# Kernel optimization log

Hardware: AMD Instinct MI355X
Metric: run time of the kernel (lower is better)

Reference implementation:

```python
import jax, jax.numpy as jnp
import numpy as np

HIDDEN = 1024
HEADS = 16
HEAD_DIM = HIDDEN // HEADS  # 64
BATCH = 2
SEQ = 2048
MASK_IDENTITY = True


def setup_inputs() -> dict:
    key = jax.random.key(0)
    ks = jax.random.split(key, 9)
    s = 1.0 / np.sqrt(HIDDEN)
    return {
        "hidden_states": jax.random.normal(ks[0], (BATCH, SEQ, HIDDEN), jnp.float32),
        "Wq": jax.random.normal(ks[1], (HIDDEN, HIDDEN), jnp.float32) * s,
        "bq": jnp.zeros((HIDDEN,), jnp.float32),
        "Wk": jax.random.normal(ks[2], (HIDDEN, HIDDEN), jnp.float32) * s,
        "bk": jnp.zeros((HIDDEN,), jnp.float32),
        "Wv": jax.random.normal(ks[3], (HIDDEN, HIDDEN), jnp.float32) * s,
        "bv": jnp.zeros((HIDDEN,), jnp.float32),
        "Wd": jax.random.normal(ks[4], (HIDDEN, HIDDEN), jnp.float32) * s,
        "bd": jnp.zeros((HIDDEN,), jnp.float32),
    }


def _split_heads(x):
    # [B, S, H*Dh] -> [B, H, S, Dh]
    b, s, _ = x.shape
    return x.reshape(b, s, HEADS, HEAD_DIM).transpose(0, 2, 1, 3)


def reference(hidden_states, Wq, bq, Wk, bk, Wv, bv, Wd, bd):
    # torch Linear: y = x @ W.T + b
    q = _split_heads(hidden_states @ Wq.T + bq)  # [B,H,S,Dh]
    k = _split_heads(hidden_states @ Wk.T + bk)
    v = _split_heads(hidden_states @ Wv.T + bv)

    scores = jnp.einsum("bhqd,bhkd->bhqk", q, k) / np.sqrt(HEAD_DIM)
    if MASK_IDENTITY:
        mask_value = -jnp.finfo(scores.dtype).max
        eye = jnp.eye(scores.shape[-1], dtype=bool)  # [S,S], broadcast over B,H
        scores = jnp.where(eye, mask_value, scores)
    probs = jax.nn.softmax(scores, axis=-1)
    ctx = jnp.einsum("bhqk,bhkd->bhqd", probs, v)  # [B,H,S,Dh]
    b, h, s, d = ctx.shape
    ctx = ctx.transpose(0, 2, 1, 3).reshape(b, s, h * d)  # [B,S,H*Dh]
    return ctx @ Wd.T + bd
```

## Files before the change

kernel.cpp:

```cpp
#include <hip/hip_runtime.h>
#include <hip/hip_bf16.h>
#include <stdint.h>

#define HIDDEN 1024
#define SEQL   2048
#define NB     2
#define NH     16
#define DH     64
#define MTOT   (NB * SEQL)
#define QKVLD  3072
#define SCALE_Q 0.18033688011112042f

typedef __bf16 bf16x8 __attribute__((ext_vector_type(8)));
typedef __bf16 bf16x4 __attribute__((ext_vector_type(4)));
typedef float  f32x4  __attribute__((ext_vector_type(4)));
typedef float  f32x16 __attribute__((ext_vector_type(16)));

__device__ __forceinline__ void gload16(const void* g, void* l) {
    __builtin_amdgcn_global_load_lds(
        (const __attribute__((address_space(1))) void*)g,
        (__attribute__((address_space(3))) void*)l, 16, 0, 0);
}
__device__ __forceinline__ float exp2fast(float x) {
    float r;
    asm("v_exp_f32 %0, %1" : "=v"(r) : "v"(x));
    return r;
}
__device__ __forceinline__ unsigned cvtpk(float lo, float hi) {
    unsigned r;
    asm("v_cvt_pk_bf16_f32 %0, %1, %2" : "=v"(r) : "v"(lo), "v"(hi));
    return r;
}
__device__ __forceinline__ void pswap(unsigned& a, unsigned& b) {
    asm volatile("v_permlane32_swap_b32 %0, %1" : "+v"(a), "+v"(b));
}
__device__ __forceinline__ void barrier_vm4() {
    asm volatile("s_waitcnt vmcnt(4)" ::: "memory");
    __builtin_amdgcn_s_barrier();
    asm volatile("" ::: "memory");
}

__global__ void prep(const float* __restrict__ H,
                     const float* __restrict__ Wq, const float* __restrict__ Wk,
                     const float* __restrict__ Wv, const float* __restrict__ Wd,
                     const float* __restrict__ bq, const float* __restrict__ bk,
                     const float* __restrict__ bv,
                     __bf16* __restrict__ Hb, __bf16* __restrict__ Wall,
                     float* __restrict__ bqkv) {
    const int bid = blockIdx.x, tid = threadIdx.x;
    if (bid < 4096) {
        int i = bid * 256 + tid;
        float4 v = reinterpret_cast<const float4*>(H)[i];
        bf16x4 o = { (__bf16)v.x, (__bf16)v.y, (__bf16)v.z, (__bf16)v.w };
        reinterpret_cast<bf16x4*>(Hb)[i] = o;
    } else if (bid < 8192) {
        int wi = bid - 4096;
        int seg = wi >> 10;
        int i = (wi & 1023) * 256 + tid;
        const float* src = seg == 0 ? Wq : seg == 1 ? Wk : seg == 2 ? Wv : Wd;
        float sc = (seg == 0) ? SCALE_Q : 1.0f;
        float4 v = reinterpret_cast<const float4*>(src)[i];
        bf16x4 o = { (__bf16)(v.x * sc), (__bf16)(v.y * sc),
                     (__bf16)(v.z * sc), (__bf16)(v.w * sc) };
        reinterpret_cast<bf16x4*>(Wall)[(size_t)seg * 262144 + i] = o;
    } else {
        for (int i = tid; i < 3072; i += 256) {
            float v = (i < 1024) ? bq[i] * SCALE_Q
                    : (i < 2048) ? bk[i - 1024] : bv[i - 2048];
            bqkv[i] = v;
        }
    }
}

__global__ __launch_bounds__(256) void transpose_v(const __bf16* __restrict__ QKV,
                                                   __bf16* __restrict__ Vt) {
    __shared__ __bf16 t[64][66];
    const int st = blockIdx.x, bh = blockIdx.y;
    const int b = bh >> 4, h = bh & 15;
    const int tid = threadIdx.x;
    const int r = tid >> 3, c = tid & 7;
    const __bf16* src = QKV + (size_t)(b * SEQL + st * 64) * QKVLD + 2048 + h * 64;
    *(int4*)&t[r][c * 8]      = *(const int4*)(src + (size_t)r * QKVLD + c * 8);
    *(int4*)&t[r + 32][c * 8] = *(const int4*)(src + (size_t)(r + 32) * QKVLD + c * 8);
    __syncthreads();
    __bf16* dst = Vt + (size_t)bh * DH * SEQL + st * 64;
    const int d = tid >> 3;
    __bf16 tmp0[8], tmp1[8];
#pragma unroll
    for (int j = 0; j < 8; ++j) {
        tmp0[j] = t[c * 8 + j][d];
        tmp1[j] = t[c * 8 + j][d + 32];
    }
    *(int4*)(dst + (size_t)d * SEQL + c * 8)        = *(int4*)tmp0;
    *(int4*)(dst + (size_t)(d + 32) * SEQL + c * 8) = *(int4*)tmp1;
}

__global__ __launch_bounds__(256) void gemm_qkv(const __bf16* __restrict__ A,
                                                const __bf16* __restrict__ Bw,
                                                const float* __restrict__ bias,
                                                __bf16* __restrict__ C) {
    __shared__ __bf16 As[3][128 * 32];
    __shared__ __bf16 Bs[3][128 * 32];
    const int K = 1024, N = QKVLD;

    int bid = blockIdx.x;
    int swz = (bid & 7) * 96 + (bid >> 3);
    const int bm = (swz & 31) * 128;
    const int bn = (swz >> 5) * 128;

    const int tid = threadIdx.x;
    const int w = tid >> 6, l = tid & 63, g = l >> 4, lc = l & 15;
    const int wr = (w >> 1) * 64, wc = (w & 1) * 64;
    const int row = tid >> 2, ch = tid & 3;

    const __bf16* Ap = A  + (size_t)(bm + row) * K + ch * 8;
    const __bf16* Bp = Bw + (size_t)(bn + row) * K + ch * 8;

    auto gstage = [&](int kt, int slot) {
        gload16(Ap + kt,                   &As[slot][w * 512]);
        gload16(Ap + kt + (size_t)64 * K,  &As[slot][2048 + w * 512]);
        gload16(Bp + kt,                   &Bs[slot][w * 512]);
        gload16(Bp + kt + (size_t)64 * K,  &Bs[slot][2048 + w * 512]);
    };

    f32x4 acc[4][4];
    const f32x4 z4 = {0.f, 0.f, 0.f, 0.f};
#pragma unroll
    for (int i = 0; i < 4; ++i)
#pragma unroll
        for (int j = 0; j < 4; ++j) acc[i][j] = z4;

    gstage(0, 0);
    gstage(32, 1);

    for (int kt = 0, it = 0; kt < K; kt += 32, ++it) {
        barrier_vm4();
        if (kt + 64 < K) gstage(kt + 64, (it + 2) % 3);

        const __bf16* Asl = &As[it % 3][0];
        const __bf16* Bsl = &Bs[it % 3][0];
        bf16x8 af[4], bfr[4];
#pragma unroll
        for (int i = 0; i < 4; ++i)
            af[i] = *(const bf16x8*)&Asl[(wr + i * 16 + lc) * 32 + g * 8];
#pragma unroll
        for (int j = 0; j < 4; ++j)
            bfr[j] = *(const bf16x8*)&Bsl[(wc + j * 16 + lc) * 32 + g * 8];
        __builtin_amdgcn_s_setprio(1);
#pragma unroll
        for (int i = 0; i < 4; ++i)
#pragma unroll
            for (int j = 0; j < 4; ++j)
                acc[i][j] = __builtin_amdgcn_mfma_f32_16x16x32_bf16(af[i], bfr[j], acc[i][j], 0, 0, 0);
        __builtin_amdgcn_s_setprio(0);
    }

#pragma unroll
    for (int i = 0; i < 4; ++i) {
        int r0 = bm + wr + i * 16 + g * 4;
#pragma unroll
        for (int j = 0; j < 4; ++j) {
            int c = bn + wc + j * 16 + lc;
            float bb = bias[c];
#pragma unroll
            for (int r = 0; r < 4; ++r)
                C[(size_t)(r0 + r) * N + c] = (__bf16)(acc[i][j][r] + bb);
        }
    }
}

__global__ __launch_bounds__(256) void gemm_out(const __bf16* __restrict__ A,
                                                const __bf16* __restrict__ Bw,
                                                const float* __restrict__ bias,
                                                float* __restrict__ Cout) {
    __shared__ __bf16 As[64 * 32];
    __shared__ __bf16 Bs[128 * 32];
    const int K = 1024, N = 1024;

    int bid = blockIdx.x;
    int swz = (bid & 7) * 64 + (bid >> 3);
    const int bm = (swz & 63) * 64;
    const int bn = (swz >> 6) * 128;

    const int tid = threadIdx.x;
    const int w = tid >> 6, l = tid & 63, g = l >> 4, lc = l & 15;
    const int wr = (w >> 1) * 32, wc = (w & 1) * 64;
    const int row = tid >> 2, ch = tid & 3;

    const __bf16* Ap = A  + (size_t)(bm + row) * K + ch * 8;
    const __bf16* Bp = Bw + (size_t)(bn + row) * K + ch * 8;
    __bf16* AsW  = &As[w * 512];
    __bf16* BsLo = &Bs[w * 512];
    __bf16* BsHi = &Bs[2048 + w * 512];

    f32x4 acc[2][4];
    const f32x4 z4 = {0.f, 0.f, 0.f, 0.f};
#pragma unroll
    for (int i = 0; i < 2; ++i)
#pragma unroll
        for (int j = 0; j < 4; ++j) acc[i][j] = z4;

    for (int kt = 0; kt < K; kt += 32) {
        gload16(Ap + kt,                   AsW);
        gload16(Bp + kt,                   BsLo);
        gload16(Bp + kt + (size_t)64 * K,  BsHi);
        __syncthreads();

        bf16x8 af[2], bfr[4];
#pragma unroll
        for (int i = 0; i < 2; ++i)
            af[i] = *(const bf16x8*)&As[(wr + i * 16 + lc) * 32 + g * 8];
#pragma unroll
        for (int j = 0; j < 4; ++j)
            bfr[j] = *(const bf16x8*)&Bs[(wc + j * 16 + lc) * 32 + g * 8];
        __builtin_amdgcn_s_setprio(1);
#pragma unroll
        for (int i = 0; i < 2; ++i)
#pragma unroll
            for (int j = 0; j < 4; ++j)
                acc[i][j] = __builtin_amdgcn_mfma_f32_16x16x32_bf16(af[i], bfr[j], acc[i][j], 0, 0, 0);
        __builtin_amdgcn_s_setprio(0);
        __syncthreads();
    }

#pragma unroll
    for (int i = 0; i < 2; ++i) {
        int r0 = bm + wr + i * 16 + g * 4;
#pragma unroll
        for (int j = 0; j < 4; ++j) {
            int c = bn + wc + j * 16 + lc;
            float bb = bias[c];
#pragma unroll
            for (int r = 0; r < 4; ++r)
                Cout[(size_t)(r0 + r) * N + c] = acc[i][j][r] + bb;
        }
    }
}

__global__ __launch_bounds__(512) void attn_kernel(const __bf16* __restrict__ QKV,
                                                   const __bf16* __restrict__ Vt,
                                                   __bf16* __restrict__ Ctx) {
    __shared__ __bf16 k_lds[3][128][64];
    __shared__ __bf16 v_lds[3][64][128];
    __shared__ float  bc[8][32];

    const int tid = threadIdx.x;
    const int w  = tid >> 6;
    const int l  = tid & 63;
    const int ql = l & 31;
    const int lh = l >> 5;

    int bid = blockIdx.x;
    int swz = (bid & 7) * 32 + (bid >> 3);
    const int qt = swz & 7, bh = swz >> 3;
    const int b = bh >> 4, hd = bh & 15;
    const int qw = qt * 256 + w * 32;

    const __bf16* Qg = QKV + (size_t)b * SEQL * QKVLD + hd * DH;
    const __bf16* Kg = Qg + 1024;
    const __bf16* Vg = Vt + (size_t)bh * DH * SEQL;

    bf16x8 qf[4];
    {
        const __bf16* qp = Qg + (size_t)(qw + ql) * QKVLD + lh * 8;
#pragma unroll
        for (int c = 0; c < 4; ++c) qf[c] = *(const bf16x8*)(qp + c * 16);
    }

    const int sr   = l >> 3;
    const int gcol = ((l & 7) ^ sr) * 8;
    const int vr  = l >> 4;
    const int vch = l & 15;
    auto stage = [&](int kb, int slot) {
        gload16(Kg + (size_t)(kb + w * 8 + sr) * QKVLD + gcol,      &k_lds[slot][w * 8][0]);
        gload16(Kg + (size_t)(kb + 64 + w * 8 + sr) * QKVLD + gcol, &k_lds[slot][64 + w * 8][0]);
        int dr0 = w * 4 + vr;
        int dr1 = 32 + w * 4 + vr;
        gload16(Vg + (size_t)dr0 * SEQL + kb + (vch ^ (dr0 & 7)) * 8, &v_lds[slot][w * 4][0]);
        gload16(Vg + (size_t)dr1 * SEQL + kb + (vch ^ (dr1 & 7)) * 8, &v_lds[slot][32 + w * 4][0]);
    };

    f32x16 o0, o1;
#pragma unroll
    for (int r = 0; r < 16; ++r) { o0[r] = 0.f; o1[r] = 0.f; }
    float l8[8];
#pragma unroll
    for (int r = 0; r < 8; ++r) l8[r] = 0.f;

    f32x16 zc;
#pragma unroll
    for (int r = 0; r < 16; ++r) zc[r] = 0.f;

    const int NT = SEQL / 128;
    const int rsw = (ql & 7) << 3;

    stage(0, 0);
    stage(128, 1);

    for (int kt = 0; kt < NT; ++kt) {
        barrier_vm4();
        if (kt + 2 < NT) stage((kt + 2) * 128, (kt + 2) % 3);

        const int buf = kt % 3;
        const int kb = kt * 128;

#pragma unroll
        for (int sub = 0; sub < 2; ++sub) {
            const int kbs = kb + sub * 64;
            const int ro  = sub * 64;

            f32x16 sA, sB;
            __builtin_amdgcn_s_setprio(1);
            {
                bf16x8 k0 = *(const bf16x8*)&k_lds[buf][ro + ql]     [(lh * 8) ^ rsw];
                bf16x8 k1 = *(const bf16x8*)&k_lds[buf][ro + 32 + ql][(lh * 8) ^ rsw];
                sA = __builtin_amdgcn_mfma_f32_32x32x16_bf16(k0, qf[0], zc, 0, 0, 0);
                sB = __builtin_amdgcn_mfma_f32_32x32x16_bf16(k1, qf[0], zc, 0, 0, 0);
            }
#pragma unroll
            for (int c = 1; c < 4; ++c) {
                bf16x8 k0 = *(const bf16x8*)&k_lds[buf][ro + ql]     [(c * 16 + lh * 8) ^ rsw];
                bf16x8 k1 = *(const bf16x8*)&k_lds[buf][ro + 32 + ql][(c * 16 + lh * 8) ^ rsw];
                sA = __builtin_amdgcn_mfma_f32_32x32x16_bf16(k0, qf[c], sA, 0, 0, 0);
                sB = __builtin_amdgcn_mfma_f32_32x32x16_bf16(k1, qf[c], sB, 0, 0, 0);
            }
            __builtin_amdgcn_s_setprio(0);

            if (kbs < qw + 32 && qw < kbs + 64) {
                const int qg = qw + ql;
#pragma unroll
                for (int i = 0; i < 16; ++i) {
                    int kg = kbs + (i & 3) + ((i >> 2) & 3) * 8 + lh * 4;
                    if (kg == qg)      sA[i] = -1e30f;
                    if (kg + 32 == qg) sB[i] = -1e30f;
                }
            }

#pragma unroll
            for (int i = 0; i < 16; ++i) sA[i] = exp2fast(sA[i]);
#pragma unroll
            for (int i = 0; i < 16; ++i) sB[i] = exp2fast(sB[i]);
#pragma unroll
            for (int i = 0; i < 8; ++i)
                l8[i] += (sA[i] + sA[i + 8]) + (sB[i] + sB[i + 8]);

            bf16x8 pa[4];
            {
                unsigned w0 = cvtpk(sA[0],  sA[1]);
                unsigned w1 = cvtpk(sA[2],  sA[3]);
                unsigned w2 = cvtpk(sA[4],  sA[5]);
                unsigned w3 = cvtpk(sA[6],  sA[7]);
                unsigned w4 = cvtpk(sA[8],  sA[9]);
                unsigned w5 = cvtpk(sA[10], sA[11]);
                unsigned w6 = cvtpk(sA[12], sA[13]);
                unsigned w7 = cvtpk(sA[14], sA[15]);
                pswap(w0, w2); pswap(w1, w3);
                pswap(w4, w6); pswap(w5, w7);
                uint4 lo4 = {w0, w1, w2, w3};
                uint4 hi4 = {w4, w5, w6, w7};
                pa[0] = *(bf16x8*)&lo4;
                pa[1] = *(bf16x8*)&hi4;
            }
            {
                unsigned w0 = cvtpk(sB[0],  sB[1]);
                unsigned w1 = cvtpk(sB[2],  sB[3]);
                unsigned w2 = cvtpk(sB[4],  sB[5]);
                unsigned w3 = cvtpk(sB[6],  sB[7]);
                unsigned w4 = cvtpk(sB[8],  sB[9]);
                unsigned w5 = cvtpk(sB[10], sB[11]);
                unsigned w6 = cvtpk(sB[12], sB[13]);
                unsigned w7 = cvtpk(sB[14], sB[15]);
                pswap(w0, w2); pswap(w1, w3);
                pswap(w4, w6); pswap(w5, w7);
                uint4 lo4 = {w0, w1, w2, w3};
                uint4 hi4 = {w4, w5, w6, w7};
                pa[2] = *(bf16x8*)&lo4;
                pa[3] = *(bf16x8*)&hi4;
            }

            __builtin_amdgcn_s_setprio(1);
#pragma unroll
            for (int s = 0; s < 2; ++s)
#pragma unroll
                for (int sl = 0; sl < 2; ++sl) {
                    const int col = sub * 64 + s * 32 + sl * 16 + lh * 8;
                    bf16x8 v0 = *(const bf16x8*)&v_lds[buf][ql]     [col ^ rsw];
                    bf16x8 v1 = *(const bf16x8*)&v_lds[buf][32 + ql][col ^ rsw];
                    o0 = __builtin_amdgcn_mfma_f32_32x32x16_bf16(pa[s * 2 + sl], v0, o0, 0, 0, 0);
                    o1 = __builtin_amdgcn_mfma_f32_32x32x16_bf16(pa[s * 2 + sl], v1, o1, 0, 0, 0);
                }
            __builtin_amdgcn_s_setprio(0);
        }
    }

    float l_r = ((l8[0] + l8[1]) + (l8[2] + l8[3]))
              + ((l8[4] + l8[5]) + (l8[6] + l8[7]));
    l_r += __shfl_xor(l_r, 32, 64);
    if (lh == 0) bc[w][ql] = 1.f / l_r;
    asm volatile("s_waitcnt lgkmcnt(0)" ::: "memory");
    __builtin_amdgcn_wave_barrier();
#pragma unroll
    for (int r = 0; r < 16; ++r) {
        int cr = (r & 3) + (r >> 2) * 8 + lh * 4;
        float iv = bc[w][cr];
        int qrow = qw + cr;
        __bf16* cp = Ctx + (size_t)(b * SEQL + qrow) * HIDDEN + hd * DH + ql;
        cp[0]  = (__bf16)(o0[r] * iv);
        cp[32] = (__bf16)(o1[r] * iv);
    }
}

extern "C" void kernel_launch(void* const* d_in, const int* in_sizes, int n_in,
                              void* d_out, int out_size, void* d_ws, size_t ws_size,
                              hipStream_t stream) {
    const float* H  = (const float*)d_in[0];
    const float* Wq = (const float*)d_in[1];
    const float* bq = (const float*)d_in[2];
    const float* Wk = (const float*)d_in[3];
    const float* bk = (const float*)d_in[4];
    const float* Wv = (const float*)d_in[5];
    const float* bv = (const float*)d_in[6];
    const float* Wd = (const float*)d_in[7];
    const float* bd = (const float*)d_in[8];
    float* out = (float*)d_out;

    char* ws = (char*)d_ws;
    const size_t MB = 1024 * 1024;
    __bf16* Hb    = (__bf16*)(ws + 0 * MB);
    __bf16* Ctx   = (__bf16*)(ws + 0 * MB);
    __bf16* Wqkvb = (__bf16*)(ws + 8 * MB);
    __bf16* Wdb   = (__bf16*)(ws + 14 * MB);
    float*  bqkv  = (float*) (ws + 16 * MB);
    __bf16* QKV   = (__bf16*)(ws + 17 * MB);
    __bf16* Vtb   = (__bf16*)(ws + 41 * MB);
    if (ws_size < 49 * MB) return;

    prep<<<8193, 256, 0, stream>>>(H, Wq, Wk, Wv, Wd, bq, bk, bv, Hb, Wqkvb, bqkv);

    gemm_qkv<<<768, 256, 0, stream>>>(Hb, Wqkvb, bqkv, QKV);

    transpose_v<<<dim3(32, 32), 256, 0, stream>>>(QKV, Vtb);

    attn_kernel<<<256, 512, 0, stream>>>(QKV, Vtb, Ctx);

    gemm_out<<<512, 256, 0, stream>>>(Ctx, Wdb, bd, out);
}
```

Before: 119.0 us.

## Widen QKV GEMM tile to 128x256 and triple-buffer output GEMM loads

After: 154.1 us. +29.5%, slower.

```diff
diff --git a/kernel.cpp b/kernel.cpp
--- a/kernel.cpp
+++ b/kernel.cpp
@@ -34,8 +34,18 @@
 __device__ __forceinline__ void pswap(unsigned& a, unsigned& b) {
     asm volatile("v_permlane32_swap_b32 %0, %1" : "+v"(a), "+v"(b));
 }
+__device__ __forceinline__ void barrier_vm3() {
+    asm volatile("s_waitcnt vmcnt(3)" ::: "memory");
+    __builtin_amdgcn_s_barrier();
+    asm volatile("" ::: "memory");
+}
 __device__ __forceinline__ void barrier_vm4() {
     asm volatile("s_waitcnt vmcnt(4)" ::: "memory");
+    __builtin_amdgcn_s_barrier();
+    asm volatile("" ::: "memory");
+}
+__device__ __forceinline__ void barrier_vm6() {
+    asm volatile("s_waitcnt vmcnt(6)" ::: "memory");
     __builtin_amdgcn_s_barrier();
     asm volatile("" ::: "memory");
 }
@@ -100,67 +110,68 @@
                                                 const float* __restrict__ bias,
                                                 __bf16* __restrict__ C) {
     __shared__ __bf16 As[3][128 * 32];
-    __shared__ __bf16 Bs[3][128 * 32];
+    __shared__ __bf16 Bs[3][256 * 32];
     const int K = 1024, N = QKVLD;
 
     int bid = blockIdx.x;
-    int swz = (bid & 7) * 96 + (bid >> 3);
+    int swz = (bid & 7) * 48 + (bid >> 3);
     const int bm = (swz & 31) * 128;
-    const int bn = (swz >> 5) * 128;
+    const int bn = (swz >> 5) * 256;
 
     const int tid = threadIdx.x;
     const int w = tid >> 6, l = tid & 63, g = l >> 4, lc = l & 15;
-    const int wr = (w >> 1) * 64, wc = (w & 1) * 64;
+    const int wm = (w >> 1) * 64, wn = (w & 1) * 128;
     const int row = tid >> 2, ch = tid & 3;
 
     const __bf16* Ap = A  + (size_t)(bm + row) * K + ch * 8;
     const __bf16* Bp = Bw + (size_t)(bn + row) * K + ch * 8;
 
     auto gstage = [&](int kt, int slot) {
-        gload16(Ap + kt,                   &As[slot][w * 512]);
-        gload16(Ap + kt + (size_t)64 * K,  &As[slot][2048 + w * 512]);
-        gload16(Bp + kt,                   &Bs[slot][w * 512]);
-        gload16(Bp + kt + (size_t)64 * K,  &Bs[slot][2048 + w * 512]);
+        gload16(Ap + kt,                    &As[slot][(w * 16) * 32]);
+        gload16(Ap + kt + (size_t)64 * K,   &As[slot][(64 + w * 16) * 32]);
+#pragma unroll
+        for (int q = 0; q < 4; ++q)
+            gload16(Bp + kt + (size_t)(64 * q) * K, &Bs[slot][(w * 16 + 64 * q) * 32]);
     };
 
-    f32x4 acc[4][4];
+    f32x4 acc[4][8];
     const f32x4 z4 = {0.f, 0.f, 0.f, 0.f};
 #pragma unroll
     for (int i = 0; i < 4; ++i)
 #pragma unroll
-        for (int j = 0; j < 4; ++j) acc[i][j] = z4;
+        for (int j = 0; j < 8; ++j) acc[i][j] = z4;
 
     gstage(0, 0);
     gstage(32, 1);
 
     for (int kt = 0, it = 0; kt < K; kt += 32, ++it) {
-        barrier_vm4();
+        barrier_vm6();
         if (kt + 64 < K) gstage(kt + 64, (it + 2) % 3);
 
         const __bf16* Asl = &As[it % 3][0];
         const __bf16* Bsl = &Bs[it % 3][0];
-        bf16x8 af[4], bfr[4];
+        bf16x8 af[4], bfr[8];
 #pragma unroll
         for (int i = 0; i < 4; ++i)
-            af[i] = *(const bf16x8*)&Asl[(wr + i * 16 + lc) * 32 + g * 8];
-#pragma unroll
-        for (int j = 0; j < 4; ++j)
-            bfr[j] = *(const bf16x8*)&Bsl[(wc + j * 16 + lc) * 32 + g * 8];
+            af[i] = *(const bf16x8*)&Asl[(wm + i * 16 + lc) * 32 + g * 8];
+#pragma unroll
+        for (int j = 0; j < 8; ++j)
+            bfr[j] = *(const bf16x8*)&Bsl[(wn + j * 16 + lc) * 32 + g * 8];
         __builtin_amdgcn_s_setprio(1);
 #pragma unroll
         for (int i = 0; i < 4; ++i)
 #pragma unroll
-            for (int j = 0; j < 4; ++j)
+            for (int j = 0; j < 8; ++j)
                 acc[i][j] = __builtin_amdgcn_mfma_f32_16x16x32_bf16(af[i], bfr[j], acc[i][j], 0, 0, 0);
         __builtin_amdgcn_s_setprio(0);
     }
 
 #pragma unroll
     for (int i = 0; i < 4; ++i) {
-        int r0 = bm + wr + i * 16 + g * 4;
-#pragma unroll
-        for (int j = 0; j < 4; ++j) {
-            int c = bn + wc + j * 16 + lc;
+        int r0 = bm + wm + i * 16 + g * 4;
+#pragma unroll
+        for (int j = 0; j < 8; ++j) {
+            int c = bn + wn + j * 16 + lc;
             float bb = bias[c];
 #pragma unroll
             for (int r = 0; r < 4; ++r)
@@ -173,8 +184,8 @@
                                                 const __bf16* __restrict__ Bw,
                                                 const float* __restrict__ bias,
                                                 float* __restrict__ Cout) {
-    __shared__ __bf16 As[64 * 32];
-    __shared__ __bf16 Bs[128 * 32];
+    __shared__ __bf16 As[3][64 * 32];
+    __shared__ __bf16 Bs[3][128 * 32];
     const int K = 1024, N = 1024;
 
     int bid = blockIdx.x;
@@ -189,9 +200,12 @@
 
     const __bf16* Ap = A  + (size_t)(bm + row) * K + ch * 8;
     const __bf16* Bp = Bw + (size_t)(bn + row) * K + ch * 8;
-    __bf16* AsW  = &As[w * 512];
-    __bf16* BsLo = &Bs[w * 512];
-    __bf16* BsHi = &Bs[2048 + w * 512];
+
+    auto gstage = [&](int kt, int slot) {
+        gload16(Ap + kt,                   &As[slot][w * 512]);
+        gload16(Bp + kt,                   &Bs[slot][w * 512]);
+        gload16(Bp + kt + (size_t)64 * K,  &Bs[slot][2048 + w * 512]);
+    };
 
     f32x4 acc[2][4];
     const f32x4 z4 = {0.f, 0.f, 0.f, 0.f};
@@ -200,19 +214,22 @@
 #pragma unroll
         for (int j = 0; j < 4; ++j) acc[i][j] = z4;
 
-    for (int kt = 0; kt < K; kt += 32) {
-        gload16(Ap + kt,                   AsW);
-        gload16(Bp + kt,                   BsLo);
-        gload16(Bp + kt + (size_t)64 * K,  BsHi);
-        __syncthreads();
-
+    gstage(0, 0);
+    gstage(32, 1);
+
+    for (int kt = 0, it = 0; kt < K; kt += 32, ++it) {
+        barrier_vm3();
+        if (kt + 64 < K) gstage(kt + 64, (it + 2) % 3);
+
+        const __bf16* Asl = &As[it % 3][0];
+        const __bf16* Bsl = &Bs[it % 3][0];
         bf16x8 af[2], bfr[4];
 #pragma unroll
         for (int i = 0; i < 2; ++i)
-            af[i] = *(const bf16x8*)&As[(wr + i * 16 + lc) * 32 + g * 8];
+            af[i] = *(const bf16x8*)&Asl[(wr + i * 16 + lc) * 32 + g * 8];
 #pragma unroll
         for (int j = 0; j < 4; ++j)
-            bfr[j] = *(const bf16x8*)&Bs[(wc + j * 16 + lc) * 32 + g * 8];
+            bfr[j] = *(const bf16x8*)&Bsl[(wc + j * 16 + lc) * 32 + g * 8];
         __builtin_amdgcn_s_setprio(1);
 #pragma unroll
         for (int i = 0; i < 2; ++i)
@@ -220,7 +237,6 @@
             for (int j = 0; j < 4; ++j)
                 acc[i][j] = __builtin_amdgcn_mfma_f32_16x16x32_bf16(af[i], bfr[j], acc[i][j], 0, 0, 0);
         __builtin_amdgcn_s_setprio(0);
-        __syncthreads();
     }
 
 #pragma unroll
@@ -437,7 +453,7 @@
 
     prep<<<8193, 256, 0, stream>>>(H, Wq, Wk, Wv, Wd, bq, bk, bv, Hb, Wqkvb, bqkv);
 
-    gemm_qkv<<<768, 256, 0, stream>>>(Hb, Wqkvb, bqkv, QKV);
+    gemm_qkv<<<384, 256, 0, stream>>>(Hb, Wqkvb, bqkv, QKV);
 
     transpose_v<<<dim3(32, 32), 256, 0, stream>>>(QKV, Vtb);
 
```
